# Kernel optimization log

Measured on AMD Instinct MI355X. Metric: run time of the kernel, lower is better.

## Reference

```python
import jax, jax.numpy as jnp
import numpy as np

B, N, C, F, P, S = 128, 32, 1024, 14, 3, 2  # batch, boxes/img, channels, fmap size, pooled size, sampling ratio
NUM_BEHAVIORS = 27


def _interp(coords, size):
    # torchvision-style bilinear weights along one axis. coords: [M]
    valid = (coords > -1.0) & (coords < size)
    c = jnp.clip(coords, 0.0, size - 1.0)
    lo = jnp.clip(jnp.floor(c).astype(jnp.int32), 0, size - 2)
    hi = lo + 1
    f = c - lo.astype(c.dtype)
    wlo = jnp.where(valid, 1.0 - f, 0.0)
    whi = jnp.where(valid, f, 0.0)
    return lo, hi, wlo, whi


def _roi_one(fm, box):
    # fm: [C,H,W], box: [4] = (x1,y1,x2,y2) in fmap coords. Returns [C,P,P].
    x1, y1, x2, y2 = box[0], box[1], box[2], box[3]
    roi_w = jnp.maximum(x2 - x1, 1.0)
    roi_h = jnp.maximum(y2 - y1, 1.0)
    bh, bw = roi_h / P, roi_w / P
    offs = (jnp.arange(S, dtype=fm.dtype) + 0.5) / S  # sample offsets within a bin
    bins = jnp.arange(P, dtype=fm.dtype)
    ys = (y1 + bins[:, None] * bh + offs[None, :] * bh).reshape(-1)  # [P*S]
    xs = (x1 + bins[:, None] * bw + offs[None, :] * bw).reshape(-1)  # [P*S]
    ylo, yhi, wylo, wyhi = _interp(ys, F)
    xlo, xhi, wxlo, wxhi = _interp(xs, F)
    # separable bilinear gather: first along H, then along W
    fy = fm[:, ylo, :] * wylo[None, :, None] + fm[:, yhi, :] * wyhi[None, :, None]  # [C,M,W]
    v = fy[:, :, xlo] * wxlo[None, None, :] + fy[:, :, xhi] * wxhi[None, None, :]    # [C,M,M]
    return v.reshape(C, P, S, P, S).mean(axis=(2, 4))


def setup_inputs() -> dict:
    key = jax.random.key(0)
    ks = jax.random.split(key, 9)
    fmap = jax.random.normal(ks[0], (B, C, F, F), dtype=jnp.float32)
    # two random corner candidates per axis -> sorted gives valid (x1,y1,x2,y2) in [0,F]
    raw = jax.random.uniform(ks[1], (B, N, 2, 2), dtype=jnp.float32) * F
    lo = raw.min(axis=2)  # [B,N,2] -> (x1,y1)
    hi = raw.max(axis=2)  # [B,N,2] -> (x2,y2)
    boxes = jnp.concatenate([lo, hi], axis=-1)  # [B,N,4]
    w_c1 = jax.random.normal(ks[2], (512, 1024), dtype=jnp.float32) * 0.03
    w_c2 = jax.random.normal(ks[3], (256, 512), dtype=jnp.float32) * 0.04
    w_fc1 = jax.random.normal(ks[4], (2304, 1024), dtype=jnp.float32) * 0.02
    b_fc1 = jax.random.normal(ks[5], (1024,), dtype=jnp.float32) * 0.01
    w_fc2 = jax.random.normal(ks[6], (1024, NUM_BEHAVIORS), dtype=jnp.float32) * 0.03
    b_fc2 = jax.random.normal(ks[7], (NUM_BEHAVIORS,), dtype=jnp.float32) * 0.01
    return {"fmap": fmap, "boxes": boxes, "w_c1": w_c1, "w_c2": w_c2,
            "w_fc1": w_fc1, "b_fc1": b_fc1, "w_fc2": w_fc2, "b_fc2": b_fc2}


def reference(fmap, boxes, w_c1, w_c2, w_fc1, b_fc1, w_fc2, b_fc2):
    boxes = jnp.clip(boxes, 0.0, float(F))  # torch.clamp(box, 0, fmap_size)
    # per-image, per-box ROIAlign without duplicating fmap per box
    pooled = jax.vmap(lambda fm, bxs: jax.vmap(lambda b: _roi_one(fm, b))(bxs))(fmap, boxes)
    pooled = jax.lax.stop_gradient(pooled)  # fmap.detach() + no_grad roi_align
    x = pooled.reshape(B * N, C, P, P)
    x = jnp.einsum('kchw,oc->kohw', x, w_c1)  # 1x1 conv, no bias
    x = jnp.einsum('kchw,oc->kohw', x, w_c2)  # 1x1 conv, no bias
    x = x.reshape(B * N, -1)                  # [K, 256*3*3] (C,H,W order as in torch .view)
    h = jax.nn.relu(x @ w_fc1 + b_fc1)        # dropout inactive (eval / deterministic ref)
    logits = h @ w_fc2 + b_fc2                # [K, num_behaviors]
    return logits
```

## Files before the change

kernel.cpp:

```cpp
#include <hip/hip_runtime.h>

typedef unsigned short ushortT;
typedef __attribute__((ext_vector_type(8))) short short8;
typedef __attribute__((ext_vector_type(4))) short short4v;
typedef __attribute__((ext_vector_type(8))) __bf16 bf16x8;
typedef __attribute__((ext_vector_type(4))) float f32x4;

__device__ __forceinline__ float bf2f(ushortT u) {
    unsigned int x = ((unsigned int)u) << 16;
    return __builtin_bit_cast(float, x);
}
__device__ __forceinline__ ushortT f2bf(float f) {
    unsigned int x = __builtin_bit_cast(unsigned int, f);
    unsigned int r = (x + 0x7FFFu + ((x >> 16) & 1u)) >> 16;
    return (ushortT)r;
}

__device__ __forceinline__ void gload_lds16(const void* g, void* l) {
    __builtin_amdgcn_global_load_lds(
        (const __attribute__((address_space(1))) void*)g,
        (__attribute__((address_space(3))) void*)l, 16, 0, 0);
}

__global__ __launch_bounds__(256, 4)
void prep_fused(const float* __restrict__ fmap,
                const float* __restrict__ w_c1, const float* __restrict__ w_c2,
                const float* __restrict__ w_fc1,
                ushortT* __restrict__ fT, float* __restrict__ wpart,
                ushortT* __restrict__ wpt)
{
    __shared__ __align__(16) char smem[33280];
    const int blk = blockIdx.x;
    const int tid = threadIdx.x;

    if (blk < 512) {
        auto w2s = reinterpret_cast<float(*)[65]>(smem);
        auto w1s = reinterpret_cast<float(*)[65]>(smem + 16640);
        const int idx = blk;
        const int o0 = (idx & 3) * 64;
        const int c0 = ((idx >> 2) & 15) * 64;
        const int z  = idx >> 6;
        const int m0 = z * 64;
        const int ty = tid >> 4, tx = tid & 15;
        float acc[4][4] = {};
        #pragma unroll
        for (int c4 = 0; c4 < 4; ++c4) {
            int id2 = c4 * 256 + tid;
            int row = id2 >> 4, f4 = id2 & 15;
            float4 v = *reinterpret_cast<const float4*>(
                w_c2 + (size_t)(o0 + row) * 512 + m0 + f4 * 4);
            w2s[row][f4*4+0] = v.x; w2s[row][f4*4+1] = v.y;
            w2s[row][f4*4+2] = v.z; w2s[row][f4*4+3] = v.w;
            float4 u = *reinterpret_cast<const float4*>(
                w_c1 + (size_t)(m0 + row) * 1024 + c0 + f4 * 4);
            w1s[row][f4*4+0] = u.x; w1s[row][f4*4+1] = u.y;
            w1s[row][f4*4+2] = u.z; w1s[row][f4*4+3] = u.w;
        }
        __syncthreads();
        for (int m = 0; m < 64; ++m) {
            float a[4], b[4];
            #pragma unroll
            for (int i = 0; i < 4; ++i) a[i] = w2s[ty*4+i][m];
            #pragma unroll
            for (int j = 0; j < 4; ++j) b[j] = w1s[m][tx*4+j];
            #pragma unroll
            for (int i = 0; i < 4; ++i)
                #pragma unroll
                for (int j = 0; j < 4; ++j) acc[i][j] = fmaf(a[i], b[j], acc[i][j]);
        }
        float* dst = wpart + (size_t)z * 262144;
        #pragma unroll
        for (int i = 0; i < 4; ++i) {
            float4 ov = { acc[i][0], acc[i][1], acc[i][2], acc[i][3] };
            *reinterpret_cast<float4*>(dst + (size_t)(o0 + ty*4 + i) * 1024 + c0 + tx*4) = ov;
        }
    } else if (blk < 1088) {
        auto tile = reinterpret_cast<float(*)[65]>(smem);
        const int idx = blk - 512;
        const int cib = idx % 36;
        const int ci0 = cib * 64;
        const int j0  = (idx / 36) * 64;
        const int hw  = ci0 >> 8;
        const int o0  = ci0 & 255;
        #pragma unroll
        for (int c4 = 0; c4 < 4; ++c4) {
            int id2 = c4 * 256 + tid;
            int row = id2 >> 4;
            int f4  = id2 & 15;
            float4 v = *reinterpret_cast<const float4*>(
                w_fc1 + (size_t)((o0 + row) * 9 + hw) * 1024 + j0 + f4 * 4);
            tile[row][f4*4+0] = v.x; tile[row][f4*4+1] = v.y;
            tile[row][f4*4+2] = v.z; tile[row][f4*4+3] = v.w;
        }
        __syncthreads();
        #pragma unroll
        for (int c4 = 0; c4 < 4; ++c4) {
            int id2 = c4 * 256 + tid;
            int j   = id2 >> 4;
            int og  = id2 & 15;
            short4v ov;
            #pragma unroll
            for (int i = 0; i < 4; ++i) ov[i] = (short)f2bf(tile[og*4+i][j]);
            *reinterpret_cast<short4v*>(wpt + (size_t)(j0 + j) * 2304 + ci0 + og*4) = ov;
        }
    } else {
        const int t  = blk - 1088;
        const int b  = t >> 4;
        const int c0 = (t & 15) << 6;

        #pragma unroll
        for (int it = 0; it < 2; ++it) {
            int item = it * 256 + tid;
            if (item < 392) {
                int c8g = item / 49;
                int q   = item - c8g * 49;
                const float* s = fmap + ((size_t)b * 1024 + c0 + c8g * 8) * 196 + q * 4;
                float4 v0 = *reinterpret_cast<const float4*>(s);
                float4 v1 = *reinterpret_cast<const float4*>(s + 196);
                float4 v2 = *reinterpret_cast<const float4*>(s + 392);
                float4 v3 = *reinterpret_cast<const float4*>(s + 588);
                float4 v4 = *reinterpret_cast<const float4*>(s + 784);
                float4 v5 = *reinterpret_cast<const float4*>(s + 980);
                float4 v6 = *reinterpret_cast<const float4*>(s + 1176);
                float4 v7 = *reinterpret_cast<const float4*>(s + 1372);
                ushortT* dbase = fT + ((size_t)b * 196 + q * 4) * 1024 + c0 + c8g * 8;
                #pragma unroll
                for (int j = 0; j < 4; ++j) {
                    short8 w = { (short)f2bf(v0[j]), (short)f2bf(v1[j]),
                                 (short)f2bf(v2[j]), (short)f2bf(v3[j]),
                                 (short)f2bf(v4[j]), (short)f2bf(v5[j]),
                                 (short)f2bf(v6[j]), (short)f2bf(v7[j]) };
                    *reinterpret_cast<short8*>(dbase + (size_t)j * 1024) = w;
                }
            }
        }
    }
}

__global__ __launch_bounds__(256)
void wct_reduce8(const float* __restrict__ part, ushortT* __restrict__ Wct_t)
{
    const int i = blockIdx.x * 256 + threadIdx.x;
    float4 s = *reinterpret_cast<const float4*>(part + (size_t)i * 4);
    #pragma unroll
    for (int z = 1; z < 8; ++z) {
        float4 v = *reinterpret_cast<const float4*>(part + (size_t)z * 262144 + (size_t)i * 4);
        s.x += v.x; s.y += v.y; s.z += v.z; s.w += v.w;
    }
    short4v ov = { (short)f2bf(s.x), (short)f2bf(s.y),
                   (short)f2bf(s.z), (short)f2bf(s.w) };
    *reinterpret_cast<short4v*>(Wct_t + (size_t)i * 4) = ov;
}

__global__ __launch_bounds__(256)
void roi_lite(const ushortT* __restrict__ fmap2, const float* __restrict__ boxes,
              ushortT* __restrict__ pooled)
{
    __shared__ ushortT tile[196][72];
    const int b   = blockIdx.x >> 2;
    const int o0  = (blockIdx.x & 3) << 6;
    const int tid = threadIdx.x;

    const ushortT* src = fmap2 + (size_t)b * 196 * 256 + o0;
    #pragma unroll
    for (int i = 0; i < 7; ++i) {
        int chunk = tid + (i << 8);
        if (chunk < 1568) {
            int p  = chunk >> 3;
            int c8 = (chunk & 7) << 3;
            short8 v = *reinterpret_cast<const short8*>(src + (size_t)p * 256 + c8);
            *reinterpret_cast<short8*>(&tile[p][c8]) = v;
        }
    }
    __syncthreads();

    const int box = tid >> 3;
    const int ch8 = (tid & 7) << 3;
    const int k   = (b << 5) + box;
    const float* bx = boxes + (size_t)k * 4;
    float x1 = fminf(fmaxf(bx[0], 0.f), 14.f);
    float y1 = fminf(fmaxf(bx[1], 0.f), 14.f);
    float x2 = fminf(fmaxf(bx[2], 0.f), 14.f);
    float y2 = fminf(fmaxf(bx[3], 0.f), 14.f);
    float bw = fmaxf(x2 - x1, 1.f) * (1.0f / 3.0f);
    float bh = fmaxf(y2 - y1, 1.f) * (1.0f / 3.0f);

    int   ylo[6], xlo[6];
    float wylo[6], wyhi[6], wxlo[6], wxhi[6];
    #pragma unroll
    for (int i = 0; i < 6; ++i) {
        float off = (i & 1) ? 0.75f : 0.25f;
        float pf  = (float)(i >> 1);
        float yc = y1 + (pf + off) * bh;
        bool  vy = (yc > -1.0f) && (yc < 14.f);
        float cy = fminf(fmaxf(yc, 0.f), 13.f);
        int   lo = (int)floorf(cy); if (lo > 12) lo = 12;
        float fy = cy - (float)lo;
        ylo[i]  = lo;
        wylo[i] = vy ? 1.f - fy : 0.f;
        wyhi[i] = vy ? fy       : 0.f;
        float xc = x1 + (pf + off) * bw;
        bool  vx = (xc > -1.0f) && (xc < 14.f);
        float cx = fminf(fmaxf(xc, 0.f), 13.f);
        int   lx = (int)floorf(cx); if (lx > 12) lx = 12;
        float fx = cx - (float)lx;
        xlo[i]  = lx;
        wxlo[i] = vx ? 1.f - fx : 0.f;
        wxhi[i] = vx ? fx       : 0.f;
    }

    float acc[3][3][8] = {};
    #pragma unroll
    for (int i = 0; i < 6; ++i) {
        #pragma unroll
        for (int j = 0; j < 6; ++j) {
            const int plo = ylo[i] * 14 + xlo[j];
            const float w00 = wylo[i] * wxlo[j];
            const float w01 = wylo[i] * wxhi[j];
            const float w10 = wyhi[i] * wxlo[j];
            const float w11 = wyhi[i] * wxhi[j];
            short8 v00 = *reinterpret_cast<const short8*>(&tile[plo][ch8]);
            short8 v01 = *reinterpret_cast<const short8*>(&tile[plo + 1][ch8]);
            short8 v10 = *reinterpret_cast<const short8*>(&tile[plo + 14][ch8]);
            short8 v11 = *reinterpret_cast<const short8*>(&tile[plo + 15][ch8]);
            #pragma unroll
            for (int c = 0; c < 8; ++c) {
                float a = acc[i >> 1][j >> 1][c];
                a = fmaf(bf2f((ushortT)v00[c]), w00, a);
                a = fmaf(bf2f((ushortT)v01[c]), w01, a);
                a = fmaf(bf2f((ushortT)v10[c]), w10, a);
                a = fmaf(bf2f((ushortT)v11[c]), w11, a);
                acc[i >> 1][j >> 1][c] = a;
            }
        }
    }

    ushortT* outp = pooled + (size_t)k * 2304 + o0 + ch8;
    #pragma unroll
    for (int p = 0; p < 3; ++p) {
        #pragma unroll
        for (int q = 0; q < 3; ++q) {
            short8 ov;
            #pragma unroll
            for (int c = 0; c < 8; ++c) ov[c] = (short)f2bf(acc[p][q][c] * 0.25f);
            *reinterpret_cast<short8*>(outp + (size_t)(p * 3 + q) * 256) = ov;
        }
    }
}

template<int RELU, int BIAS>
__global__ __launch_bounds__(256, 2)
void gemm_mfma(const ushortT* __restrict__ A, const ushortT* __restrict__ Bt,
               ushortT* __restrict__ C, const float* __restrict__ bias,
               int M, int N, int K)
{
    __shared__ ushortT As[2][128 * 64];
    const int tid  = threadIdx.x;
    const int wid  = tid >> 6;
    const int lane = tid & 63;
    const int ncolb = N >> 6;
    const int nblk  = (M >> 7) * ncolb;
    const int cpx   = nblk >> 3;
    const int i     = blockIdx.x;
    const int w     = (i & 7) * cpx + (i >> 3);
    const size_t row0 = (size_t)(w / ncolb) * 128;
    const size_t col0 = (size_t)(w % ncolb) * 64;

    const ushortT* agbase = A + row0 * K;
    auto stage = [&](int k0, int buf) {
        #pragma unroll
        for (int q = 0; q < 4; ++q) {
            int id  = q * 256 + tid;
            int row = id >> 3;
            int kcs = (id & 7) ^ (row & 7);
            gload_lds16(agbase + (size_t)row * K + k0 + kcs * 8,
                        As[buf] + id * 8);
        }
    };

    const int fr = lane & 15;
    const int kq = lane >> 4;
    const int rx = fr & 7;
    auto lda = [&](const ushortT* Ab, int m, int s) -> bf16x8 {
        const int r = m * 16 + fr;
        const int c = (s << 2) + kq;
        return *reinterpret_cast<const bf16x8*>(&Ab[(r << 6) + ((c ^ rx) << 3)]);
    };

    const ushortT* bbase = Bt + (col0 + wid * 16 + fr) * (size_t)K + kq * 8;
    auto loadB2 = [&](int k0, bf16x8& r0, bf16x8& r1) {
        r0 = *reinterpret_cast<const bf16x8*>(bbase + k0);
        r1 = *reinterpret_cast<const bf16x8*>(bbase + k0 + 32);
    };

    f32x4 acc[8];
    #pragma unroll
    for (int m = 0; m < 8; ++m) acc[m] = (f32x4){0,0,0,0};

    auto domfma = [&](const ushortT* Ab, bf16x8 b0, bf16x8 b1) {
        #pragma unroll
        for (int m = 0; m < 8; ++m) {
            acc[m] = __builtin_amdgcn_mfma_f32_16x16x32_bf16(lda(Ab, m, 0), b0, acc[m], 0, 0, 0);
            acc[m] = __builtin_amdgcn_mfma_f32_16x16x32_bf16(lda(Ab, m, 1), b1, acc[m], 0, 0, 0);
        }
    };

    const int nsteps = K >> 6;
    bf16x8 bA0, bA1, bB0, bB1;
    stage(0, 0);
    loadB2(0, bA0, bA1);
    __syncthreads();

    #pragma unroll 1
    for (int s = 0; s < (nsteps >> 1); ++s) {
        const int t = 2 * s;
        if (t + 1 < nsteps) { stage((t + 1) * 64, 1); loadB2((t + 1) * 64, bB0, bB1); }
        domfma(As[0], bA0, bA1);
        __syncthreads();
        if (t + 2 < nsteps) { stage((t + 2) * 64, 0); loadB2((t + 2) * 64, bA0, bA1); }
        domfma(As[1], bB0, bB1);
        __syncthreads();
    }

    const int orow = kq * 4;
    const size_t col = col0 + wid * 16 + fr;
    float bv = 0.f;
    if (BIAS) bv = bias[col];
    #pragma unroll
    for (int m = 0; m < 8; ++m) {
        const size_t rbase = row0 + m * 16 + orow;
        #pragma unroll
        for (int j = 0; j < 4; ++j) {
            float v = acc[m][j] + bv;
            if (RELU) v = fmaxf(v, 0.f);
            C[(rbase + j) * N + col] = f2bf(v);
        }
    }
}

__global__ __launch_bounds__(256)
void fc2_kernel(const ushortT* __restrict__ h, const float* __restrict__ w,
                const float* __restrict__ bias, float* __restrict__ out)
{
    __shared__ float   Wsm[128][32];
    __shared__ ushortT Hs[16][136];
    const int tid  = threadIdx.x;
    const int row0 = blockIdx.x * 16;
    const int r    = tid >> 4;
    const int jg   = tid & 15;
    float accx = 0.f, accy = 0.f;

    const int kk2  = tid >> 1;
    const int half = tid & 1;

    for (int k0 = 0; k0 < 1024; k0 += 128) {
        if (half == 0) {
            #pragma unroll
            for (int j = 0; j < 14; ++j)
                Wsm[kk2][j] = w[(size_t)(k0 + kk2) * 27 + j];
        } else {
            #pragma unroll
            for (int j = 14; j < 27; ++j)
                Wsm[kk2][j] = w[(size_t)(k0 + kk2) * 27 + j];
            #pragma unroll
            for (int j = 27; j < 32; ++j) Wsm[kk2][j] = 0.f;
        }
        {
            int hr = tid >> 4, hc = tid & 15;
            short8 v = *reinterpret_cast<const short8*>(
                h + (size_t)(row0 + hr) * 1024 + k0 + hc * 8);
            *reinterpret_cast<short8*>(&Hs[hr][hc * 8]) = v;
        }
        __syncthreads();
        #pragma unroll 8
        for (int kk = 0; kk < 128; ++kk) {
            float  hv = bf2f(Hs[r][kk]);
            float2 wv = *reinterpret_cast<const float2*>(&Wsm[kk][jg * 2]);
            accx = fmaf(hv, wv.x, accx);
            accy = fmaf(hv, wv.y, accy);
        }
        __syncthreads();
    }
    const int j0 = jg * 2;
    float* op = out + (size_t)(row0 + r) * 27;
    if (j0 < 27)     op[j0]     = accx + bias[j0];
    if (j0 + 1 < 27) op[j0 + 1] = accy + bias[j0 + 1];
}

extern "C" void kernel_launch(void* const* d_in, const int* in_sizes, int n_in,
                              void* d_out, int out_size, void* d_ws, size_t ws_size,
                              hipStream_t stream)
{
    (void)in_sizes; (void)n_in; (void)out_size; (void)ws_size;
    const float* fmap  = (const float*)d_in[0];
    const float* boxes = (const float*)d_in[1];
    const float* w_c1  = (const float*)d_in[2];
    const float* w_c2  = (const float*)d_in[3];
    const float* w_fc1 = (const float*)d_in[4];
    const float* b_fc1 = (const float*)d_in[5];
    const float* w_fc2 = (const float*)d_in[6];
    const float* b_fc2 = (const float*)d_in[7];
    float* out = (float*)d_out;

    char* ws = (char*)d_ws;
    size_t off = 0;
    ushortT* fmapT  = (ushortT*)(ws + off); off += (size_t)25088 * 1024 * 2;
    ushortT* fmap2  = (ushortT*)(ws + off); off += (size_t)25088 * 256 * 2;
    ushortT* pooled = (ushortT*)(ws + off); off += (size_t)4096 * 2304 * 2;
    ushortT* hbuf   = (ushortT*)(ws + off); off += (size_t)4096 * 1024 * 2;
    ushortT* Wct_t  = (ushortT*)(ws + off); off += (size_t)256 * 1024 * 2;
    ushortT* wp_t   = (ushortT*)(ws + off); off += (size_t)1024 * 2304 * 2;
    float*   wpart  = (float*)(ws + off);   off += (size_t)8 * 262144 * 4;

    hipLaunchKernelGGL(prep_fused, dim3(3136), dim3(256), 0, stream,
                       fmap, w_c1, w_c2, w_fc1, fmapT, wpart, wp_t);
    hipLaunchKernelGGL(wct_reduce8, dim3(256), dim3(256), 0, stream, wpart, Wct_t);

    hipLaunchKernelGGL((gemm_mfma<0,0>), dim3(784), dim3(256), 0, stream,
                       fmapT, Wct_t, fmap2, (const float*)nullptr, 25088, 256, 1024);
    hipLaunchKernelGGL(roi_lite, dim3(512), dim3(256), 0, stream, fmap2, boxes, pooled);
    hipLaunchKernelGGL((gemm_mfma<1,1>), dim3(512), dim3(256), 0, stream,
                       pooled, wp_t, hbuf, b_fc1, 4096, 1024, 2304);
    hipLaunchKernelGGL(fc2_kernel, dim3(256), dim3(256), 0, stream,
                       hbuf, w_fc2, b_fc2, out);
}
```

Measured before the change: 154.6 us.

## Fuse fmap transpose/bf16 conversion into direct MFMA 1x1 conv kernel

Removes the separate pass that transposed the fp32 feature map into a bf16 channel-last buffer. A new conv_direct kernel instead streams fp32 fmap tiles straight into LDS with async global-to-LDS loads and swizzled addressing. It converts them to bf16 on the fly while building MFMA operands, with double-buffered staging of both fmap and weight tiles. This saves a full write and re-read of a ~51MB intermediate, but LDS traffic rises because fp32 tiles are staged and A fragments are gathered element by element.

```diff
diff --git a/kernel.cpp b/kernel.cpp
--- a/kernel.cpp
+++ b/kernel.cpp
@@ -22,12 +22,10 @@
         (__attribute__((address_space(3))) void*)l, 16, 0, 0);
 }
 
-__global__ __launch_bounds__(256, 4)
-void prep_fused(const float* __restrict__ fmap,
-                const float* __restrict__ w_c1, const float* __restrict__ w_c2,
+__global__ __launch_bounds__(256)
+void prep_fused(const float* __restrict__ w_c1, const float* __restrict__ w_c2,
                 const float* __restrict__ w_fc1,
-                ushortT* __restrict__ fT, float* __restrict__ wpart,
-                ushortT* __restrict__ wpt)
+                float* __restrict__ wpart, ushortT* __restrict__ wpt)
 {
     __shared__ __align__(16) char smem[33280];
     const int blk = blockIdx.x;
@@ -74,7 +72,7 @@
             float4 ov = { acc[i][0], acc[i][1], acc[i][2], acc[i][3] };
             *reinterpret_cast<float4*>(dst + (size_t)(o0 + ty*4 + i) * 1024 + c0 + tx*4) = ov;
         }
-    } else if (blk < 1088) {
+    } else {
         auto tile = reinterpret_cast<float(*)[65]>(smem);
         const int idx = blk - 512;
         const int cib = idx % 36;
@@ -103,37 +101,6 @@
             for (int i = 0; i < 4; ++i) ov[i] = (short)f2bf(tile[og*4+i][j]);
             *reinterpret_cast<short4v*>(wpt + (size_t)(j0 + j) * 2304 + ci0 + og*4) = ov;
         }
-    } else {
-        const int t  = blk - 1088;
-        const int b  = t >> 4;
-        const int c0 = (t & 15) << 6;
-
-        #pragma unroll
-        for (int it = 0; it < 2; ++it) {
-            int item = it * 256 + tid;
-            if (item < 392) {
-                int c8g = item / 49;
-                int q   = item - c8g * 49;
-                const float* s = fmap + ((size_t)b * 1024 + c0 + c8g * 8) * 196 + q * 4;
-                float4 v0 = *reinterpret_cast<const float4*>(s);
-                float4 v1 = *reinterpret_cast<const float4*>(s + 196);
-                float4 v2 = *reinterpret_cast<const float4*>(s + 392);
-                float4 v3 = *reinterpret_cast<const float4*>(s + 588);
-                float4 v4 = *reinterpret_cast<const float4*>(s + 784);
-                float4 v5 = *reinterpret_cast<const float4*>(s + 980);
-                float4 v6 = *reinterpret_cast<const float4*>(s + 1176);
-                float4 v7 = *reinterpret_cast<const float4*>(s + 1372);
-                ushortT* dbase = fT + ((size_t)b * 196 + q * 4) * 1024 + c0 + c8g * 8;
-                #pragma unroll
-                for (int j = 0; j < 4; ++j) {
-                    short8 w = { (short)f2bf(v0[j]), (short)f2bf(v1[j]),
-                                 (short)f2bf(v2[j]), (short)f2bf(v3[j]),
-                                 (short)f2bf(v4[j]), (short)f2bf(v5[j]),
-                                 (short)f2bf(v6[j]), (short)f2bf(v7[j]) };
-                    *reinterpret_cast<short8*>(dbase + (size_t)j * 1024) = w;
-                }
-            }
-        }
     }
 }
 
@@ -150,6 +117,107 @@
     short4v ov = { (short)f2bf(s.x), (short)f2bf(s.y),
                    (short)f2bf(s.z), (short)f2bf(s.w) };
     *reinterpret_cast<short4v*>(Wct_t + (size_t)i * 4) = ov;
+}
+
+__global__ __launch_bounds__(256, 2)
+void conv_direct(const float* __restrict__ fmap, const ushortT* __restrict__ Wct_t,
+                 ushortT* __restrict__ fmap2)
+{
+    __shared__ float   Pf[2][64 * 64];
+    __shared__ ushortT Wb[2][128 * 64];
+    const int tid  = threadIdx.x;
+    const int wid  = tid >> 6;
+    const int lane = tid & 63;
+    const int fr   = lane & 15;
+    const int kq   = lane >> 4;
+
+    const int i   = blockIdx.x;
+    const int w   = (i & 7) * 98 + (i >> 3);
+    const int gp0 = (w >> 1) * 64;
+    const int o0  = (w & 1) * 128;
+
+    const float* psrc[4];
+    const ushortT* wsrc[4];
+    #pragma unroll
+    for (int q = 0; q < 4; ++q) {
+        int id = q * 256 + tid;
+        int c  = id >> 4;
+        int js = id & 15;
+        int x  = (c + 4 * (c >> 3)) & 15;
+        int j  = js ^ x;
+        int gg = (gp0 >> 2) + j;
+        int bb = gg / 49;
+        int p4g = gg - bb * 49;
+        psrc[q] = fmap + ((size_t)bb * 1024 + c) * 196 + p4g * 4;
+        int row = id >> 3;
+        int kcs = (id & 7) ^ (row & 7);
+        wsrc[q] = Wct_t + (size_t)(o0 + row) * 1024 + kcs * 8;
+    }
+
+    auto stage = [&](int k0, int buf) {
+        #pragma unroll
+        for (int q = 0; q < 4; ++q) {
+            int id = q * 256 + tid;
+            gload_lds16(psrc[q] + (size_t)k0 * 196, (char*)&Pf[buf][0] + id * 16);
+            gload_lds16(wsrc[q] + k0,               (char*)&Wb[buf][0] + id * 16);
+        }
+    };
+
+    const int rx = fr & 7;
+    auto wread = [&](const ushortT* WB, int n, int ks) -> bf16x8 {
+        int wo = wid * 32 + n * 16 + fr;
+        int c4 = ((ks << 2) + kq) ^ rx;
+        return *reinterpret_cast<const bf16x8*>(&WB[(wo << 6) + (c4 << 3)]);
+    };
+    const int p4b = fr >> 2, pr = fr & 3;
+    auto aread = [&](const float* PB, int m, int ks) -> bf16x8 {
+        const int p4 = m * 4 + p4b;
+        bf16x8 a;
+        #pragma unroll
+        for (int i2 = 0; i2 < 8; ++i2) {
+            int x = (i2 + 12 * kq) & 15;
+            int c = ks * 32 + kq * 8 + i2;
+            a[i2] = (__bf16)PB[(c << 6) + ((p4 ^ x) << 2) + pr];
+        }
+        return a;
+    };
+
+    f32x4 acc[4][2];
+    #pragma unroll
+    for (int m = 0; m < 4; ++m) { acc[m][0] = (f32x4){0,0,0,0}; acc[m][1] = (f32x4){0,0,0,0}; }
+
+    stage(0, 0);
+    __syncthreads();
+
+    #pragma unroll 1
+    for (int t = 0; t < 16; ++t) {
+        const int cur = t & 1, nxt = cur ^ 1;
+        if (t < 15) stage((t + 1) * 64, nxt);
+        bf16x8 w00 = wread(Wb[cur], 0, 0), w01 = wread(Wb[cur], 0, 1);
+        bf16x8 w10 = wread(Wb[cur], 1, 0), w11 = wread(Wb[cur], 1, 1);
+        #pragma unroll
+        for (int m = 0; m < 4; ++m) {
+            bf16x8 a0 = aread(Pf[cur], m, 0);
+            acc[m][0] = __builtin_amdgcn_mfma_f32_16x16x32_bf16(a0, w00, acc[m][0], 0, 0, 0);
+            acc[m][1] = __builtin_amdgcn_mfma_f32_16x16x32_bf16(a0, w10, acc[m][1], 0, 0, 0);
+            bf16x8 a1 = aread(Pf[cur], m, 1);
+            acc[m][0] = __builtin_amdgcn_mfma_f32_16x16x32_bf16(a1, w01, acc[m][0], 0, 0, 0);
+            acc[m][1] = __builtin_amdgcn_mfma_f32_16x16x32_bf16(a1, w11, acc[m][1], 0, 0, 0);
+        }
+        __syncthreads();
+    }
+
+    #pragma unroll
+    for (int m = 0; m < 4; ++m) {
+        const int gp = gp0 + m * 16 + kq * 4;
+        #pragma unroll
+        for (int n = 0; n < 2; ++n) {
+            const int o = o0 + wid * 32 + n * 16 + fr;
+            #pragma unroll
+            for (int jj = 0; jj < 4; ++jj)
+                fmap2[(size_t)(gp + jj) * 256 + o] = f2bf(acc[m][n][jj]);
+        }
+    }
 }
 
 __global__ __launch_bounds__(256)
@@ -404,7 +472,6 @@
 
     char* ws = (char*)d_ws;
     size_t off = 0;
-    ushortT* fmapT  = (ushortT*)(ws + off); off += (size_t)25088 * 1024 * 2;
     ushortT* fmap2  = (ushortT*)(ws + off); off += (size_t)25088 * 256 * 2;
     ushortT* pooled = (ushortT*)(ws + off); off += (size_t)4096 * 2304 * 2;
     ushortT* hbuf   = (ushortT*)(ws + off); off += (size_t)4096 * 1024 * 2;
@@ -412,15 +479,15 @@
     ushortT* wp_t   = (ushortT*)(ws + off); off += (size_t)1024 * 2304 * 2;
     float*   wpart  = (float*)(ws + off);   off += (size_t)8 * 262144 * 4;
 
-    hipLaunchKernelGGL(prep_fused, dim3(3136), dim3(256), 0, stream,
-                       fmap, w_c1, w_c2, w_fc1, fmapT, wpart, wp_t);
-    hipLaunchKernelGGL(wct_reduce8, dim3(256), dim3(256), 0, stream, wpart, Wct_t);
-
-    hipLaunchKernelGGL((gemm_mfma<0,0>), dim3(784), dim3(256), 0, stream,
-                       fmapT, Wct_t, fmap2, (const float*)nullptr, 25088, 256, 1024);
-    hipLaunchKernelGGL(roi_lite, dim3(512), dim3(256), 0, stream, fmap2, boxes, pooled);
+    hipLaunchKernelGGL(prep_fused,  dim3(1088), dim3(256), 0, stream,
+                       w_c1, w_c2, w_fc1, wpart, wp_t);
+    hipLaunchKernelGGL(wct_reduce8, dim3(256),  dim3(256), 0, stream, wpart, Wct_t);
+
+    hipLaunchKernelGGL(conv_direct, dim3(784),  dim3(256), 0, stream,
+                       fmap, Wct_t, fmap2);
+    hipLaunchKernelGGL(roi_lite,    dim3(512),  dim3(256), 0, stream, fmap2, boxes, pooled);
     hipLaunchKernelGGL((gemm_mfma<1,1>), dim3(512), dim3(256), 0, stream,
                        pooled, wp_t, hbuf, b_fc1, 4096, 1024, 2304);
-    hipLaunchKernelGGL(fc2_kernel, dim3(256), dim3(256), 0, stream,
+    hipLaunchKernelGGL(fc2_kernel,  dim3(256),  dim3(256), 0, stream,
                        hbuf, w_fc2, b_fc2, out);
 }
```

Result: faster. 136.6 us (-11.6%).
